# Optimization experiments

Measured on AMD Instinct MI355X. Metric: run time of the kernel, lower is better.

Reference implementation:

```python
import jax, jax.numpy as jnp
import numpy as np

N = 500          # number of brain regions (nodes)
T = 20000        # Euler integration steps
DT = 0.05        # integration step size
SQDT = float(np.sqrt(DT))
NOISE_STD = 0.02 # state-noise amplitude


def setup_inputs() -> dict:
    key = jax.random.key(0)
    ks = jax.random.split(key, 7)
    sc = jax.random.uniform(ks[0], (N, N), dtype=jnp.float32)
    sc = 0.5 * (sc + sc.T)
    sc = sc / jnp.sum(sc, axis=1, keepdims=True)  # row-normalized SC (deg_i = 1)
    x0 = 0.1 * jax.random.normal(ks[1], (N,), dtype=jnp.float32)
    y0 = 0.1 * jax.random.normal(ks[2], (N,), dtype=jnp.float32)
    a = jax.random.uniform(ks[3], (N,), dtype=jnp.float32)           # bifurcation param per node, in [0,1)
    omega = 0.1 + 0.4 * jax.random.uniform(ks[4], (N,), dtype=jnp.float32)  # intrinsic angular frequency
    noise = NOISE_STD * jax.random.normal(ks[5], (T, N, 2), dtype=jnp.float32)
    g = 0.05 * jnp.ones((1,), dtype=jnp.float32)                     # global coupling
    return {"sc": sc, "x0": x0, "y0": y0, "a": a, "omega": omega, "noise": noise, "g": g}


def reference(sc, x0, y0, a, omega, noise, g):
    """Coupled Hopf oscillators, Euler-Maruyama over T steps.
    Returns the x-trajectory [T, N]."""
    deg = jnp.sum(sc, axis=1)  # [N], in-strength for diffusive coupling

    def step(carry, nz):
        x, y = carry                       # [N], [N]
        r2 = x * x + y * y                 # |z|^2
        cx = sc @ x - deg * x              # diffusive coupling sum_j SC_ij (x_j - x_i)
        cy = sc @ y - deg * y
        dx = (a - r2) * x - omega * y + g * cx
        dy = (a - r2) * y + omega * x + g * cy
        xn = x + DT * dx + SQDT * nz[:, 0]
        yn = y + DT * dy + SQDT * nz[:, 1]
        return (xn, yn), xn

    _, xs = jax.lax.scan(step, (x0, y0), noise)
    return xs  # [T, N]
```

## Files before the change

kernel.cpp:

```cpp
#include <hip/hip_runtime.h>

#define NN    500
#define TT    20000
#define NPAD  512
#define NBLK  8
#define NROW  64
#define TPB   512
#define RPT   4
#define CPT   16
#define DTC   0.05f
#define SQDTC 0.22360679774997896f

typedef unsigned int u32x4 __attribute__((ext_vector_type(4)));

__device__ __forceinline__ void store_coh_u128(u32x4* p, u32x4 v) {
    asm volatile("global_store_dwordx4 %0, %1, off sc0 sc1" :: "v"(p), "v"(v) : "memory");
}
__device__ __forceinline__ u32x4 load_coh_u128(const u32x4* p) {
    u32x4 v;
    asm volatile("global_load_dwordx4 %0, %1, off sc0 sc1\n\t"
                 "s_waitcnt vmcnt(0)" : "=v"(v) : "v"(p) : "memory");
    return v;
}

__global__ __launch_bounds__(512) void hopf_init_ws(u32x4* pub) {
    int i = blockIdx.x * blockDim.x + threadIdx.x;
    if (i < 2 * NPAD) pub[i] = (u32x4){0u, 0u, 0u, 0u};
}

__global__ __launch_bounds__(TPB) void hopf_main(
    const float* __restrict__ sc, const float* __restrict__ x0,
    const float* __restrict__ y0, const float* __restrict__ aa,
    const float* __restrict__ om, const float* __restrict__ noise,
    const float* __restrict__ gg, float* __restrict__ out,
    u32x4* __restrict__ pub)
{
    const int tid  = threadIdx.x;
    const int blk  = blockIdx.x;
    const int cgrp = tid & 31;
    const int rgrp = tid >> 5;
    const int r0   = blk * NROW + rgrp * RPT;

    __shared__ __align__(16) float2 xy[NPAD];

    float scr[RPT][CPT];
#pragma unroll
    for (int r = 0; r < RPT; ++r) {
        int row = r0 + r;
#pragma unroll
        for (int c = 0; c < CPT; ++c) {
            int col = cgrp + 32 * c;
            scr[r][c] = (row < NN && col < NN) ? sc[row * NN + col] : 0.0f;
        }
    }

    float dsum[RPT];
#pragma unroll
    for (int r = 0; r < RPT; ++r) {
        float s = 0.f;
#pragma unroll
        for (int c = 0; c < CPT; ++c) s += scr[r][c];
        dsum[r] = s;
    }
#pragma unroll
    for (int m = 16; m >= 1; m >>= 1) {
#pragma unroll
        for (int r = 0; r < RPT; ++r) dsum[r] += __shfl_xor(dsum[r], m, 32);
    }

#pragma unroll
    for (int r = 0; r < RPT; ++r)
#pragma unroll
        for (int c = 0; c < CPT; ++c)
            asm volatile("" : "+v"(scr[r][c]));

    float a_i = 0.f, om_i = 0.f, deg_i = 0.f;
    int myrow = -1;
    if (cgrp < RPT) {
        int row = r0 + cgrp;
        deg_i = (cgrp == 0) ? dsum[0] : (cgrp == 1) ? dsum[1]
              : (cgrp == 2) ? dsum[2] : dsum[3];
        if (row < NN) { myrow = row; a_i = aa[row]; om_i = om[row]; }
    }
    const float g = gg[0];

    xy[tid] = (tid < NN) ? make_float2(x0[tid], y0[tid]) : make_float2(0.f, 0.f);
    __syncthreads();

    float2 nz = make_float2(0.f, 0.f);
    if (myrow >= 0) nz = *(const float2*)(noise + 2 * (size_t)myrow);

    for (int t = 0; t < TT; ++t) {
        float2 nz_next = make_float2(0.f, 0.f);
        if (myrow >= 0 && t + 1 < TT)
            nz_next = *(const float2*)(noise + (size_t)(t + 1) * (2 * NN) + 2 * (size_t)myrow);

        float2 acc[RPT];
#pragma unroll
        for (int r = 0; r < RPT; ++r) acc[r] = make_float2(0.f, 0.f);
#pragma unroll
        for (int c = 0; c < CPT; ++c) {
            float2 w = xy[cgrp + 32 * c];
#pragma unroll
            for (int r = 0; r < RPT; ++r) {
                acc[r].x += scr[r][c] * w.x;
                acc[r].y += scr[r][c] * w.y;
            }
        }
#pragma unroll
        for (int m = 16; m >= 1; m >>= 1) {
#pragma unroll
            for (int r = 0; r < RPT; ++r) {
                acc[r].x += __shfl_xor(acc[r].x, m, 32);
                acc[r].y += __shfl_xor(acc[r].y, m, 32);
            }
        }

        if (myrow >= 0) {
            float sx = (cgrp == 0) ? acc[0].x : (cgrp == 1) ? acc[1].x
                     : (cgrp == 2) ? acc[2].x : acc[3].x;
            float sy = (cgrp == 0) ? acc[0].y : (cgrp == 1) ? acc[1].y
                     : (cgrp == 2) ? acc[2].y : acc[3].y;
            float2 cur = xy[myrow];
            float r2 = cur.x * cur.x + cur.y * cur.y;
            float cx = sx - deg_i * cur.x;
            float cy = sy - deg_i * cur.y;
            float dx = (a_i - r2) * cur.x - om_i * cur.y + g * cx;
            float dy = (a_i - r2) * cur.y + om_i * cur.x + g * cy;
            float xn = cur.x + DTC * dx + SQDTC * nz.x;
            float yn = cur.y + DTC * dy + SQDTC * nz.y;
            out[(size_t)t * NN + myrow] = xn;
            u32x4 pkt = { __float_as_uint(xn), (unsigned)(t + 1),
                          __float_as_uint(yn), (unsigned)(t + 1) };
            store_coh_u128(&pub[(size_t)(t & 1) * NPAD + myrow], pkt);
        }
        nz = nz_next;

        if (t == TT - 1) break;

        __syncthreads();

        if (tid < NN) {
            const u32x4* slot = &pub[(size_t)(t & 1) * NPAD + tid];
            u32x4 v;
            do {
                v = load_coh_u128(slot);
            } while ((int)v.y < t + 1 || (int)v.w < t + 1);
            xy[tid] = make_float2(__uint_as_float(v.x), __uint_as_float(v.z));
        }
        __syncthreads();
    }
}

extern "C" void kernel_launch(void* const* d_in, const int* in_sizes, int n_in,
                              void* d_out, int out_size, void* d_ws, size_t ws_size,
                              hipStream_t stream) {
    const float* sc = (const float*)d_in[0];
    const float* x0 = (const float*)d_in[1];
    const float* y0 = (const float*)d_in[2];
    const float* aa = (const float*)d_in[3];
    const float* om = (const float*)d_in[4];
    const float* nz = (const float*)d_in[5];
    const float* gg = (const float*)d_in[6];
    float* out = (float*)d_out;

    u32x4* pub = (u32x4*)d_ws;

    hipLaunchKernelGGL(hopf_init_ws, dim3(2), dim3(512), 0, stream, pub);
    hipLaunchKernelGGL(hopf_main, dim3(NBLK), dim3(TPB), 0, stream,
                       sc, x0, y0, aa, om, nz, gg, out, pub);
}
```

Baseline: 42.64 ms.

## Double-buffer shared state, pipeline flag polling, and split rows over 1024 threads

After: 62.35 ms. +46.2%, slower.

```diff
diff --git a/kernel.cpp b/kernel.cpp
--- a/kernel.cpp
+++ b/kernel.cpp
@@ -5,8 +5,8 @@
 #define NPAD  512
 #define NBLK  8
 #define NROW  64
-#define TPB   512
-#define RPT   4
+#define TPB   1024
+#define RPT   2
 #define CPT   16
 #define DTC   0.05f
 #define SQDTC 0.22360679774997896f
@@ -23,7 +23,7 @@
     return v;
 }
 
-__global__ __launch_bounds__(512) void hopf_init_ws(u32x4* pub) {
+__global__ __launch_bounds__(1024) void hopf_init_ws(u32x4* pub) {
     int i = blockIdx.x * blockDim.x + threadIdx.x;
     if (i < 2 * NPAD) pub[i] = (u32x4){0u, 0u, 0u, 0u};
 }
@@ -41,7 +41,7 @@
     const int rgrp = tid >> 5;
     const int r0   = blk * NROW + rgrp * RPT;
 
-    __shared__ __align__(16) float2 xy[NPAD];
+    __shared__ __align__(16) float2 xy[2][NPAD];
 
     float scr[RPT][CPT];
 #pragma unroll
@@ -78,19 +78,22 @@
     int myrow = -1;
     if (cgrp < RPT) {
         int row = r0 + cgrp;
-        deg_i = (cgrp == 0) ? dsum[0] : (cgrp == 1) ? dsum[1]
-              : (cgrp == 2) ? dsum[2] : dsum[3];
+        deg_i = (cgrp == 0) ? dsum[0] : dsum[1];
         if (row < NN) { myrow = row; a_i = aa[row]; om_i = om[row]; }
     }
     const float g = gg[0];
 
-    xy[tid] = (tid < NN) ? make_float2(x0[tid], y0[tid]) : make_float2(0.f, 0.f);
+    xy[0][tid < NPAD ? tid : 0] = make_float2(0.f, 0.f);
+    xy[1][tid < NPAD ? tid : 0] = make_float2(0.f, 0.f);
+    __syncthreads();
+    if (tid < NN) xy[0][tid] = make_float2(x0[tid], y0[tid]);
     __syncthreads();
 
     float2 nz = make_float2(0.f, 0.f);
     if (myrow >= 0) nz = *(const float2*)(noise + 2 * (size_t)myrow);
 
     for (int t = 0; t < TT; ++t) {
+        const int p = t & 1;
         float2 nz_next = make_float2(0.f, 0.f);
         if (myrow >= 0 && t + 1 < TT)
             nz_next = *(const float2*)(noise + (size_t)(t + 1) * (2 * NN) + 2 * (size_t)myrow);
@@ -100,7 +103,7 @@
         for (int r = 0; r < RPT; ++r) acc[r] = make_float2(0.f, 0.f);
 #pragma unroll
         for (int c = 0; c < CPT; ++c) {
-            float2 w = xy[cgrp + 32 * c];
+            float2 w = xy[p][cgrp + 32 * c];
 #pragma unroll
             for (int r = 0; r < RPT; ++r) {
                 acc[r].x += scr[r][c] * w.x;
@@ -117,11 +120,9 @@
         }
 
         if (myrow >= 0) {
-            float sx = (cgrp == 0) ? acc[0].x : (cgrp == 1) ? acc[1].x
-                     : (cgrp == 2) ? acc[2].x : acc[3].x;
-            float sy = (cgrp == 0) ? acc[0].y : (cgrp == 1) ? acc[1].y
-                     : (cgrp == 2) ? acc[2].y : acc[3].y;
-            float2 cur = xy[myrow];
+            float sx = (cgrp == 0) ? acc[0].x : acc[1].x;
+            float sy = (cgrp == 0) ? acc[0].y : acc[1].y;
+            float2 cur = xy[p][myrow];
             float r2 = cur.x * cur.x + cur.y * cur.y;
             float cx = sx - deg_i * cur.x;
             float cy = sy - deg_i * cur.y;
@@ -129,24 +130,33 @@
             float dy = (a_i - r2) * cur.y + om_i * cur.x + g * cy;
             float xn = cur.x + DTC * dx + SQDTC * nz.x;
             float yn = cur.y + DTC * dy + SQDTC * nz.y;
-            out[(size_t)t * NN + myrow] = xn;
             u32x4 pkt = { __float_as_uint(xn), (unsigned)(t + 1),
                           __float_as_uint(yn), (unsigned)(t + 1) };
-            store_coh_u128(&pub[(size_t)(t & 1) * NPAD + myrow], pkt);
+            store_coh_u128(&pub[(size_t)p * NPAD + myrow], pkt);
+            out[(size_t)t * NN + myrow] = xn;
         }
         nz = nz_next;
 
         if (t == TT - 1) break;
 
-        __syncthreads();
-
         if (tid < NN) {
-            const u32x4* slot = &pub[(size_t)(t & 1) * NPAD + tid];
-            u32x4 v;
-            do {
-                v = load_coh_u128(slot);
-            } while ((int)v.y < t + 1 || (int)v.w < t + 1);
-            xy[tid] = make_float2(__uint_as_float(v.x), __uint_as_float(v.z));
+            const u32x4* slot = &pub[(size_t)p * NPAD + tid];
+            const int need = t + 1;
+            u32x4 va;
+            asm volatile("global_load_dwordx4 %0, %1, off sc0 sc1\n\t"
+                         "global_load_dwordx4 %0, %1, off sc0 sc1"
+                         : "=v"(va) : "v"(slot) : "memory");
+            for (;;) {
+                asm volatile("s_waitcnt vmcnt(1)" ::: "memory");
+                __builtin_amdgcn_sched_barrier(0);
+                if ((int)va.y >= need && (int)va.w >= need) break;
+                asm volatile("global_load_dwordx4 %0, %1, off sc0 sc1"
+                             : "+v"(va) : "v"(slot) : "memory");
+            }
+            asm volatile("s_waitcnt vmcnt(0)" ::: "memory");
+            __builtin_amdgcn_sched_barrier(0);
+            if ((int)va.y < need || (int)va.w < need) va = load_coh_u128(slot);
+            xy[p ^ 1][tid] = make_float2(__uint_as_float(va.x), __uint_as_float(va.z));
         }
         __syncthreads();
     }
@@ -166,7 +176,7 @@
 
     u32x4* pub = (u32x4*)d_ws;
 
-    hipLaunchKernelGGL(hopf_init_ws, dim3(2), dim3(512), 0, stream, pub);
+    hipLaunchKernelGGL(hopf_init_ws, dim3(1), dim3(1024), 0, stream, pub);
     hipLaunchKernelGGL(hopf_main, dim3(NBLK), dim3(TPB), 0, stream,
                        sc, x0, y0, aa, om, nz, gg, out, pub);
 }
```

## Double-buffer shared state, drop one barrier per step, prefetch noise chunks

Applied to the files above, without the earlier changes.

After: 47.28 ms. 1.11x slower.

```diff
diff --git a/kernel.cpp b/kernel.cpp
--- a/kernel.cpp
+++ b/kernel.cpp
@@ -8,6 +8,7 @@
 #define TPB   512
 #define RPT   4
 #define CPT   16
+#define CHUNK 64
 #define DTC   0.05f
 #define SQDTC 0.22360679774997896f
 
@@ -23,9 +24,27 @@
     return v;
 }
 
-__global__ __launch_bounds__(512) void hopf_init_ws(u32x4* pub) {
+__global__ __launch_bounds__(1024) void hopf_init_ws(u32x4* pub) {
     int i = blockIdx.x * blockDim.x + threadIdx.x;
     if (i < 2 * NPAD) pub[i] = (u32x4){0u, 0u, 0u, 0u};
+}
+
+__device__ __forceinline__ void load_noise_chunk(const float* noise, int blk, int tid,
+                                                 int cb0, float2 (*nbuf)[64]) {
+    const int stp = tid >> 3;
+    const int rb  = (tid & 7) * 8;
+    int g = cb0 + stp; if (g > TT - 1) g = TT - 1;
+    const char* base = (const char*)noise + (size_t)g * (NN * 2 * 4);
+    u32x4 v[4];
+#pragma unroll
+    for (int i = 0; i < 4; ++i) {
+        int row = blk * NROW + rb + 2 * i;
+        if (row > NN - 2) row = NN - 2;
+        v[i] = *(const u32x4*)(base + (size_t)row * 8);
+    }
+#pragma unroll
+    for (int i = 0; i < 4; ++i)
+        *(u32x4*)&nbuf[stp][rb + 2 * i] = v[i];
 }
 
 __global__ __launch_bounds__(TPB) void hopf_main(
@@ -41,7 +60,8 @@
     const int rgrp = tid >> 5;
     const int r0   = blk * NROW + rgrp * RPT;
 
-    __shared__ __align__(16) float2 xy[NPAD];
+    __shared__ __align__(16) float2 xy[2][NPAD];
+    __shared__ __align__(16) float2 nbuf[2][CHUNK][64];
 
     float scr[RPT][CPT];
 #pragma unroll
@@ -83,24 +103,29 @@
         if (row < NN) { myrow = row; a_i = aa[row]; om_i = om[row]; }
     }
     const float g = gg[0];
-
-    xy[tid] = (tid < NN) ? make_float2(x0[tid], y0[tid]) : make_float2(0.f, 0.f);
+    const int ri = rgrp * RPT + cgrp;
+
+    if (tid < NPAD) {
+        xy[0][tid] = (tid < NN) ? make_float2(x0[tid], y0[tid]) : make_float2(0.f, 0.f);
+        xy[1][tid] = make_float2(0.f, 0.f);
+    }
+    load_noise_chunk(noise, blk, tid, 0, nbuf[0]);
     __syncthreads();
 
-    float2 nz = make_float2(0.f, 0.f);
-    if (myrow >= 0) nz = *(const float2*)(noise + 2 * (size_t)myrow);
-
     for (int t = 0; t < TT; ++t) {
-        float2 nz_next = make_float2(0.f, 0.f);
-        if (myrow >= 0 && t + 1 < TT)
-            nz_next = *(const float2*)(noise + (size_t)(t + 1) * (2 * NN) + 2 * (size_t)myrow);
+        const int p  = t & 1;
+        const int so = t & (CHUNK - 1);
+        const int cb = (t >> 6) & 1;
+
+        float2 nz = make_float2(0.f, 0.f);
+        if (myrow >= 0) nz = nbuf[cb][so][ri];
 
         float2 acc[RPT];
 #pragma unroll
         for (int r = 0; r < RPT; ++r) acc[r] = make_float2(0.f, 0.f);
 #pragma unroll
         for (int c = 0; c < CPT; ++c) {
-            float2 w = xy[cgrp + 32 * c];
+            float2 w = xy[p][cgrp + 32 * c];
 #pragma unroll
             for (int r = 0; r < RPT; ++r) {
                 acc[r].x += scr[r][c] * w.x;
@@ -116,38 +141,46 @@
             }
         }
 
+        float xn = 0.f;
         if (myrow >= 0) {
             float sx = (cgrp == 0) ? acc[0].x : (cgrp == 1) ? acc[1].x
                      : (cgrp == 2) ? acc[2].x : acc[3].x;
             float sy = (cgrp == 0) ? acc[0].y : (cgrp == 1) ? acc[1].y
                      : (cgrp == 2) ? acc[2].y : acc[3].y;
-            float2 cur = xy[myrow];
+            float2 cur = xy[p][myrow];
             float r2 = cur.x * cur.x + cur.y * cur.y;
             float cx = sx - deg_i * cur.x;
             float cy = sy - deg_i * cur.y;
             float dx = (a_i - r2) * cur.x - om_i * cur.y + g * cx;
             float dy = (a_i - r2) * cur.y + om_i * cur.x + g * cy;
-            float xn = cur.x + DTC * dx + SQDTC * nz.x;
+            xn = cur.x + DTC * dx + SQDTC * nz.x;
             float yn = cur.y + DTC * dy + SQDTC * nz.y;
-            out[(size_t)t * NN + myrow] = xn;
             u32x4 pkt = { __float_as_uint(xn), (unsigned)(t + 1),
                           __float_as_uint(yn), (unsigned)(t + 1) };
-            store_coh_u128(&pub[(size_t)(t & 1) * NPAD + myrow], pkt);
-        }
-        nz = nz_next;
-
-        if (t == TT - 1) break;
-
-        __syncthreads();
-
+            store_coh_u128(&pub[(size_t)p * NPAD + myrow], pkt);
+        }
+
+        if (t == TT - 1) {
+            if (myrow >= 0) out[(size_t)t * NN + myrow] = xn;
+            break;
+        }
+
+        u32x4 va;
         if (tid < NN) {
-            const u32x4* slot = &pub[(size_t)(t & 1) * NPAD + tid];
-            u32x4 v;
+            const u32x4* slot = &pub[(size_t)p * NPAD + tid];
             do {
-                v = load_coh_u128(slot);
-            } while ((int)v.y < t + 1 || (int)v.w < t + 1);
-            xy[tid] = make_float2(__uint_as_float(v.x), __uint_as_float(v.z));
-        }
+                va = load_coh_u128(slot);
+            } while ((int)va.y < t + 1 || (int)va.w < t + 1);
+        }
+
+        if (myrow >= 0) out[(size_t)t * NN + myrow] = xn;
+
+        if (tid < NN)
+            xy[p ^ 1][tid] = make_float2(__uint_as_float(va.x), __uint_as_float(va.z));
+
+        if (so == CHUNK - 1)
+            load_noise_chunk(noise, blk, tid, t + 1, nbuf[cb ^ 1]);
+
         __syncthreads();
     }
 }
@@ -166,7 +199,7 @@
 
     u32x4* pub = (u32x4*)d_ws;
 
-    hipLaunchKernelGGL(hopf_init_ws, dim3(2), dim3(512), 0, stream, pub);
+    hipLaunchKernelGGL(hopf_init_ws, dim3(1), dim3(1024), 0, stream, pub);
     hipLaunchKernelGGL(hopf_main, dim3(NBLK), dim3(TPB), 0, stream,
                        sc, x0, y0, aa, om, nz, gg, out, pub);
 }
```

## Load noise via scalar loads and double-buffer coherent spin-wait polling

Applied to the files above, without the earlier changes.

New measurement: 59.23 ms. +38.9%, slower.

```diff
diff --git a/kernel.cpp b/kernel.cpp
--- a/kernel.cpp
+++ b/kernel.cpp
@@ -11,7 +11,8 @@
 #define DTC   0.05f
 #define SQDTC 0.22360679774997896f
 
-typedef unsigned int u32x4 __attribute__((ext_vector_type(4)));
+typedef unsigned int u32x4  __attribute__((ext_vector_type(4)));
+typedef unsigned int u32x16 __attribute__((ext_vector_type(16)));
 
 __device__ __forceinline__ void store_coh_u128(u32x4* p, u32x4 v) {
     asm volatile("global_store_dwordx4 %0, %1, off sc0 sc1" :: "v"(p), "v"(v) : "memory");
@@ -23,7 +24,14 @@
     return v;
 }
 
-__global__ __launch_bounds__(512) void hopf_init_ws(u32x4* pub) {
+__device__ __forceinline__ float pick8(const u32x16& s, int k, int off) {
+    unsigned r = (k < 4)
+        ? ((k < 2) ? (k == 0 ? s[0 + off] : s[2 + off]) : (k == 2 ? s[4 + off] : s[6 + off]))
+        : ((k < 6) ? (k == 4 ? s[8 + off] : s[10 + off]) : (k == 6 ? s[12 + off] : s[14 + off]));
+    return __uint_as_float(r);
+}
+
+__global__ __launch_bounds__(1024) void hopf_init_ws(u32x4* pub) {
     int i = blockIdx.x * blockDim.x + threadIdx.x;
     if (i < 2 * NPAD) pub[i] = (u32x4){0u, 0u, 0u, 0u};
 }
@@ -84,16 +92,24 @@
     }
     const float g = gg[0];
 
+    int nb_ = blk * NROW + 8 * (tid >> 6);
+    if (nb_ > NN - 8) nb_ = NN - 8;
+    const int nb = __builtin_amdgcn_readfirstlane(nb_);
+    const float* nwav = noise + 2 * (size_t)nb;
+    const int ri8 = myrow - nb;
+
     xy[tid] = (tid < NN) ? make_float2(x0[tid], y0[tid]) : make_float2(0.f, 0.f);
     __syncthreads();
 
-    float2 nz = make_float2(0.f, 0.f);
-    if (myrow >= 0) nz = *(const float2*)(noise + 2 * (size_t)myrow);
+    u32x4 va = {0u, 0u, 0u, 0u}, vb = {0u, 0u, 0u, 0u};
 
     for (int t = 0; t < TT; ++t) {
-        float2 nz_next = make_float2(0.f, 0.f);
-        if (myrow >= 0 && t + 1 < TT)
-            nz_next = *(const float2*)(noise + (size_t)(t + 1) * (2 * NN) + 2 * (size_t)myrow);
+        const int p = t & 1;
+
+        u32x16 sg;
+        unsigned noff = (unsigned)t * (unsigned)(NN * 2 * 4);
+        asm volatile("s_load_dwordx16 %0, %1, %2"
+                     : "=&s"(sg) : "s"(nwav), "s"(noff) : "memory");
 
         float2 acc[RPT];
 #pragma unroll
@@ -115,41 +131,59 @@
                 acc[r].y += __shfl_xor(acc[r].y, m, 32);
             }
         }
+
+        asm volatile("s_waitcnt lgkmcnt(0)" : "+s"(sg) :: "memory");
 
         if (myrow >= 0) {
             float sx = (cgrp == 0) ? acc[0].x : (cgrp == 1) ? acc[1].x
                      : (cgrp == 2) ? acc[2].x : acc[3].x;
             float sy = (cgrp == 0) ? acc[0].y : (cgrp == 1) ? acc[1].y
                      : (cgrp == 2) ? acc[2].y : acc[3].y;
+            float nx = pick8(sg, ri8, 0);
+            float ny = pick8(sg, ri8, 1);
             float2 cur = xy[myrow];
             float r2 = cur.x * cur.x + cur.y * cur.y;
             float cx = sx - deg_i * cur.x;
             float cy = sy - deg_i * cur.y;
             float dx = (a_i - r2) * cur.x - om_i * cur.y + g * cx;
             float dy = (a_i - r2) * cur.y + om_i * cur.x + g * cy;
-            float xn = cur.x + DTC * dx + SQDTC * nz.x;
-            float yn = cur.y + DTC * dy + SQDTC * nz.y;
+            float xn = cur.x + DTC * dx + SQDTC * nx;
+            float yn = cur.y + DTC * dy + SQDTC * ny;
             out[(size_t)t * NN + myrow] = xn;
             u32x4 pkt = { __float_as_uint(xn), (unsigned)(t + 1),
                           __float_as_uint(yn), (unsigned)(t + 1) };
-            store_coh_u128(&pub[(size_t)(t & 1) * NPAD + myrow], pkt);
-        }
-        nz = nz_next;
+            store_coh_u128(&pub[(size_t)p * NPAD + myrow], pkt);
+        }
 
         if (t == TT - 1) break;
 
         __syncthreads();
 
         if (tid < NN) {
-            const u32x4* slot = &pub[(size_t)(t & 1) * NPAD + tid];
-            u32x4 v;
-            do {
-                v = load_coh_u128(slot);
-            } while ((int)v.y < t + 1 || (int)v.w < t + 1);
-            xy[tid] = make_float2(__uint_as_float(v.x), __uint_as_float(v.z));
+            const u32x4* slot = &pub[(size_t)p * NPAD + tid];
+            const int need = t + 1;
+            asm volatile("global_load_dwordx4 %0, %2, off sc0 sc1\n\t"
+                         "global_load_dwordx4 %1, %2, off sc0 sc1"
+                         : "+v"(va), "+v"(vb) : "v"(slot) : "memory");
+            u32x4 res;
+            for (;;) {
+                asm volatile("s_waitcnt vmcnt(1)" ::: "memory");
+                __builtin_amdgcn_sched_barrier(0);
+                if ((int)va.y >= need && (int)va.w >= need) { res = va; break; }
+                asm volatile("global_load_dwordx4 %0, %1, off sc0 sc1"
+                             : "+v"(va) : "v"(slot) : "memory");
+                asm volatile("s_waitcnt vmcnt(1)" ::: "memory");
+                __builtin_amdgcn_sched_barrier(0);
+                if ((int)vb.y >= need && (int)vb.w >= need) { res = vb; break; }
+                asm volatile("global_load_dwordx4 %0, %1, off sc0 sc1"
+                             : "+v"(vb) : "v"(slot) : "memory");
+            }
+            xy[tid] = make_float2(__uint_as_float(res.x), __uint_as_float(res.z));
         }
         __syncthreads();
     }
+
+    asm volatile("" :: "v"(va), "v"(vb));
 }
 
 extern "C" void kernel_launch(void* const* d_in, const int* in_sizes, int n_in,
@@ -166,7 +200,7 @@
 
     u32x4* pub = (u32x4*)d_ws;
 
-    hipLaunchKernelGGL(hopf_init_ws, dim3(2), dim3(512), 0, stream, pub);
+    hipLaunchKernelGGL(hopf_init_ws, dim3(1), dim3(1024), 0, stream, pub);
     hipLaunchKernelGGL(hopf_main, dim3(NBLK), dim3(TPB), 0, stream,
                        sc, x0, y0, aa, om, nz, gg, out, pub);
 }
```
